# Performance work log

Measured on AMD Instinct MI355X. Metric: run time of the kernel, lower is better.

## Reference

```python
import jax, jax.numpy as jnp
import numpy as np

SEQ_LEN = 16384
IN_DIM = 2048
STATE_DIM = 2048


def setup_inputs() -> dict:
    key = jax.random.key(0)
    k_xs, k_lam, k_win, k_c, k_d = jax.random.split(key, 5)
    xs = jax.random.normal(k_xs, (SEQ_LEN, IN_DIM), dtype=jnp.float32)
    # diagonal state-transition values in (0, 1) for stability
    lam = jax.random.uniform(k_lam, (STATE_DIM,), dtype=jnp.float32)
    w_in = jax.random.normal(k_win, (STATE_DIM, IN_DIM), dtype=jnp.float32) / np.float32(np.sqrt(IN_DIM))
    c_out = jax.random.normal(k_c, (IN_DIM, STATE_DIM), dtype=jnp.float32) / np.float32(np.sqrt(STATE_DIM))
    d_skip = jax.random.normal(k_d, (IN_DIM,), dtype=jnp.float32)
    return {"xs": xs, "lam": lam, "w_in": w_in, "c_out": c_out, "d_skip": d_skip}


def _ssm_cell(a, b):
    # Faithful replication of BaseSSMLayer.ssm_cell (including its use of
    # matrix_pow_i * matrix_pow_i for the first component, exactly as in source).
    matrix_pow_i, bx_i = a
    matrix_pow_j, bx_j = b
    return (matrix_pow_i * matrix_pow_i, matrix_pow_j * bx_i + bx_j)


def reference(xs, lam, w_in, c_out, d_skip):
    seq_len = xs.shape[0]
    # discretize: broadcast diagonal lambda over the sequence -> [L, N]
    lambda_elements = jnp.broadcast_to(lam, (seq_len, lam.shape[0]))
    # preprocess_inputs: vmap(w_in @ x) == xs @ w_in.T  -> [L, N]
    w_in_xs = jnp.einsum('li,ni->ln', xs, w_in)
    _, hs = jax.lax.associative_scan(_ssm_cell, (lambda_elements, w_in_xs))
    # postprocess: y_t = C h_t + D * x_t  -> [L, in_dim]
    return jnp.einsum('ln,on->lo', hs, c_out) + xs * d_skip
```

## Files before the change

### kernel.cpp

```cpp
#include <hip/hip_runtime.h>
#include <hip/hip_bf16.h>

#define SEQ   16384
#define DIM   2048
#define CHUNK 256
#define NCHUNK (SEQ / CHUNK)

typedef __attribute__((ext_vector_type(8))) short  short8;
typedef __attribute__((ext_vector_type(4))) short  short4v;
typedef __attribute__((ext_vector_type(4))) float  floatx4;

static __device__ __forceinline__ float bf2f(short s) {
    return __uint_as_float(((unsigned)(unsigned short)s) << 16);
}
static __device__ __forceinline__ short f2bf(float f) {
    unsigned u = __float_as_uint(f);
    u += 0x7fff + ((u >> 16) & 1);
    return (short)(u >> 16);
}

__global__ void cast_kernel(const float* __restrict__ in, short* __restrict__ out, int n4) {
    int i = blockIdx.x * blockDim.x + threadIdx.x;
    if (i >= n4) return;
    float4 v = ((const float4*)in)[i];
    short4v s;
    s.x = f2bf(v.x); s.y = f2bf(v.y); s.z = f2bf(v.z); s.w = f2bf(v.w);
    ((short4v*)out)[i] = s;
}

template<int FUSE>
__global__ __launch_bounds__(256, 2)
void gemm_bt(const short* __restrict__ A, const short* __restrict__ B,
             short* __restrict__ Cbf, float* __restrict__ Cf,
             const float* __restrict__ xs, const float* __restrict__ dskip)
{
    constexpr int K = DIM;
    __shared__ alignas(16) short As[128 * 32];
    __shared__ alignas(16) short Bs[128 * 32];

    const int tid = threadIdx.x;
    const int m0  = blockIdx.y * 128;
    const int n0  = blockIdx.x * 128;

    const int c0 = tid, c1 = tid + 256;
    const short* ga0 = A + (size_t)(m0 + (c0 >> 2)) * K + (c0 & 3) * 8;
    const short* ga1 = A + (size_t)(m0 + (c1 >> 2)) * K + (c1 & 3) * 8;
    const short* gb0 = B + (size_t)(n0 + (c0 >> 2)) * K + (c0 & 3) * 8;
    const short* gb1 = B + (size_t)(n0 + (c1 >> 2)) * K + (c1 & 3) * 8;
    short* la0 = &As[c0 * 8];
    short* la1 = &As[c1 * 8];
    short* lb0 = &Bs[c0 * 8];
    short* lb1 = &Bs[c1 * 8];

    const int lane = tid & 63;
    const int wv   = tid >> 6;
    const int wm   = (wv >> 1) * 64;
    const int wn   = (wv & 1) * 64;
    const int l16  = lane & 15;
    const int quad = lane >> 4;

    floatx4 acc[4][4] = {};

    for (int kk = 0; kk < K; kk += 32) {
        __builtin_amdgcn_global_load_lds(ga0 + kk, la0, 16, 0, 0);
        __builtin_amdgcn_global_load_lds(ga1 + kk, la1, 16, 0, 0);
        __builtin_amdgcn_global_load_lds(gb0 + kk, lb0, 16, 0, 0);
        __builtin_amdgcn_global_load_lds(gb1 + kk, lb1, 16, 0, 0);
        __syncthreads();

        short8 aV[4], bV[4];
        #pragma unroll
        for (int i = 0; i < 4; i++)
            aV[i] = *(const short8*)&As[(wm + i * 16 + l16) * 32 + quad * 8];
        #pragma unroll
        for (int i = 0; i < 4; i++)
            bV[i] = *(const short8*)&Bs[(wn + i * 16 + l16) * 32 + quad * 8];

        #pragma unroll
        for (int mi = 0; mi < 4; mi++)
            #pragma unroll
            for (int ni = 0; ni < 4; ni++)
                acc[mi][ni] = __builtin_amdgcn_mfma_f32_16x16x32_bf16(
                    aV[mi], bV[ni], acc[mi][ni], 0, 0, 0);
        __syncthreads();
    }

    if (FUSE == 0) {
        #pragma unroll
        for (int mi = 0; mi < 4; mi++) {
            int rb = m0 + wm + mi * 16 + quad * 4;
            #pragma unroll
            for (int ni = 0; ni < 4; ni++) {
                int cc = n0 + wn + ni * 16 + l16;
                #pragma unroll
                for (int r = 0; r < 4; r++)
                    Cbf[(size_t)(rb + r) * DIM + cc] = f2bf(acc[mi][ni][r]);
            }
        }
    } else {
        float dsk[4];
        #pragma unroll
        for (int ni = 0; ni < 4; ni++) dsk[ni] = dskip[n0 + wn + ni * 16 + l16];
        #pragma unroll
        for (int mi = 0; mi < 4; mi++) {
            int rb = m0 + wm + mi * 16 + quad * 4;
            #pragma unroll
            for (int ni = 0; ni < 4; ni++) {
                int cc = n0 + wn + ni * 16 + l16;
                #pragma unroll
                for (int r = 0; r < 4; r++) {
                    size_t idx = (size_t)(rb + r) * DIM + cc;
                    Cf[idx] = acc[mi][ni][r] + xs[idx] * dsk[ni];
                }
            }
        }
    }
}

__global__ void scan_pass1(const short* __restrict__ bx, const float* __restrict__ lam,
                           float* __restrict__ blockLast)
{
    int n     = blockIdx.x * 256 + threadIdx.x;
    int chunk = blockIdx.y;
    float lm  = lam[n];
    const short* p = bx + (size_t)chunk * CHUNK * DIM + n;
    float h = 0.f;
    #pragma unroll 8
    for (int i = 0; i < CHUNK; i++)
        h = fmaf(lm, h, bf2f(p[(size_t)i * DIM]));
    blockLast[(size_t)chunk * DIM + n] = h;
}

__global__ void scan_pass2(float* __restrict__ blockLast, const float* __restrict__ lam)
{
    int n    = blockIdx.x * 256 + threadIdx.x;
    float lm = lam[n];
    float p  = lm;
    #pragma unroll
    for (int i = 0; i < 8; i++) p = p * p;
    float carry = 0.f;
    for (int c = 0; c < NCHUNK; c++) {
        float t = blockLast[(size_t)c * DIM + n];
        blockLast[(size_t)c * DIM + n] = carry;
        carry = fmaf(p, carry, t);
    }
}

__global__ void scan_pass3(short* __restrict__ bxh, const float* __restrict__ lam,
                           const float* __restrict__ carry)
{
    int n     = blockIdx.x * 256 + threadIdx.x;
    int chunk = blockIdx.y;
    float lm  = lam[n];
    float h   = carry[(size_t)chunk * DIM + n];
    short* p  = bxh + (size_t)chunk * CHUNK * DIM + n;
    #pragma unroll 8
    for (int i = 0; i < CHUNK; i++) {
        h = fmaf(lm, h, bf2f(p[(size_t)i * DIM]));
        p[(size_t)i * DIM] = f2bf(h);
    }
}

extern "C" void kernel_launch(void* const* d_in, const int* in_sizes, int n_in,
                              void* d_out, int out_size, void* d_ws, size_t ws_size,
                              hipStream_t stream)
{
    const float* xs    = (const float*)d_in[0];
    const float* lam   = (const float*)d_in[1];
    const float* w_in  = (const float*)d_in[2];
    const float* c_out = (const float*)d_in[3];
    const float* dskip = (const float*)d_in[4];
    float* out = (float*)d_out;

    char*  ws    = (char*)d_ws;
    short* bxh   = (short*)ws;
    short* w_bf  = (short*)(ws + (size_t)64 * 1024 * 1024);
    short* c_bf  = (short*)(ws + (size_t)72 * 1024 * 1024);
    float* blkl  = (float*)(ws + (size_t)80 * 1024 * 1024);
    short* xs_bf = (short*)d_out;

    cast_kernel<<<SEQ * DIM / 4 / 256, 256, 0, stream>>>(xs, xs_bf, SEQ * DIM / 4);
    cast_kernel<<<DIM * DIM / 4 / 256, 256, 0, stream>>>(w_in, w_bf, DIM * DIM / 4);
    cast_kernel<<<DIM * DIM / 4 / 256, 256, 0, stream>>>(c_out, c_bf, DIM * DIM / 4);

    dim3 ggrid(DIM / 128, SEQ / 128);
    gemm_bt<0><<<ggrid, 256, 0, stream>>>(xs_bf, w_bf, bxh, nullptr, nullptr, nullptr);

    dim3 sgrid(DIM / 256, NCHUNK);
    scan_pass1<<<sgrid, 256, 0, stream>>>(bxh, lam, blkl);
    scan_pass2<<<DIM / 256, 256, 0, stream>>>(blkl, lam);
    scan_pass3<<<sgrid, 256, 0, stream>>>(bxh, lam, blkl);

    gemm_bt<1><<<ggrid, 256, 0, stream>>>(bxh, c_bf, nullptr, out, xs, dskip);
}
```

Baseline: 629.3 us.

## Double-buffer GEMM LDS tiles and vectorize chunked scan passes

The GEMM now double-buffers its LDS tiles, issuing the next k-slice's global-to-LDS loads before computing the current one, and drops one barrier per iteration. The three scan passes now have each thread handle four state columns with vectorized bf16 and float4 accesses. The chunk size is halved so the coarser per-thread work still gives enough blocks. Double buffering doubles LDS use per block, and the single-barrier scheme relies on global_load_lds completion being covered by the barrier wait. The scan grid is still small (2x128 blocks).

```diff
diff --git a/kernel.cpp b/kernel.cpp
--- a/kernel.cpp
+++ b/kernel.cpp
@@ -3,7 +3,7 @@
 
 #define SEQ   16384
 #define DIM   2048
-#define CHUNK 256
+#define CHUNK 128
 #define NCHUNK (SEQ / CHUNK)
 
 typedef __attribute__((ext_vector_type(8))) short  short8;
@@ -35,8 +35,9 @@
              const float* __restrict__ xs, const float* __restrict__ dskip)
 {
     constexpr int K = DIM;
-    __shared__ alignas(16) short As[128 * 32];
-    __shared__ alignas(16) short Bs[128 * 32];
+    constexpr int ITERS = K / 32;
+    __shared__ alignas(16) short As[2][128 * 32];
+    __shared__ alignas(16) short Bs[2][128 * 32];
 
     const int tid = threadIdx.x;
     const int m0  = blockIdx.y * 128;
@@ -47,10 +48,6 @@
     const short* ga1 = A + (size_t)(m0 + (c1 >> 2)) * K + (c1 & 3) * 8;
     const short* gb0 = B + (size_t)(n0 + (c0 >> 2)) * K + (c0 & 3) * 8;
     const short* gb1 = B + (size_t)(n0 + (c1 >> 2)) * K + (c1 & 3) * 8;
-    short* la0 = &As[c0 * 8];
-    short* la1 = &As[c1 * 8];
-    short* lb0 = &Bs[c0 * 8];
-    short* lb1 = &Bs[c1 * 8];
 
     const int lane = tid & 63;
     const int wv   = tid >> 6;
@@ -61,20 +58,31 @@
 
     floatx4 acc[4][4] = {};
 
-    for (int kk = 0; kk < K; kk += 32) {
-        __builtin_amdgcn_global_load_lds(ga0 + kk, la0, 16, 0, 0);
-        __builtin_amdgcn_global_load_lds(ga1 + kk, la1, 16, 0, 0);
-        __builtin_amdgcn_global_load_lds(gb0 + kk, lb0, 16, 0, 0);
-        __builtin_amdgcn_global_load_lds(gb1 + kk, lb1, 16, 0, 0);
+    __builtin_amdgcn_global_load_lds(ga0, &As[0][c0 * 8], 16, 0, 0);
+    __builtin_amdgcn_global_load_lds(ga1, &As[0][c1 * 8], 16, 0, 0);
+    __builtin_amdgcn_global_load_lds(gb0, &Bs[0][c0 * 8], 16, 0, 0);
+    __builtin_amdgcn_global_load_lds(gb1, &Bs[0][c1 * 8], 16, 0, 0);
+
+    for (int it = 0; it < ITERS; ++it) {
+        const int cur = it & 1;
         __syncthreads();
 
+        if (it + 1 < ITERS) {
+            const int kk = (it + 1) * 32;
+            const int nxt = cur ^ 1;
+            __builtin_amdgcn_global_load_lds(ga0 + kk, &As[nxt][c0 * 8], 16, 0, 0);
+            __builtin_amdgcn_global_load_lds(ga1 + kk, &As[nxt][c1 * 8], 16, 0, 0);
+            __builtin_amdgcn_global_load_lds(gb0 + kk, &Bs[nxt][c0 * 8], 16, 0, 0);
+            __builtin_amdgcn_global_load_lds(gb1 + kk, &Bs[nxt][c1 * 8], 16, 0, 0);
+        }
+
         short8 aV[4], bV[4];
         #pragma unroll
         for (int i = 0; i < 4; i++)
-            aV[i] = *(const short8*)&As[(wm + i * 16 + l16) * 32 + quad * 8];
+            aV[i] = *(const short8*)&As[cur][(wm + i * 16 + l16) * 32 + quad * 8];
         #pragma unroll
         for (int i = 0; i < 4; i++)
-            bV[i] = *(const short8*)&Bs[(wn + i * 16 + l16) * 32 + quad * 8];
+            bV[i] = *(const short8*)&Bs[cur][(wn + i * 16 + l16) * 32 + quad * 8];
 
         #pragma unroll
         for (int mi = 0; mi < 4; mi++)
@@ -82,7 +90,6 @@
             for (int ni = 0; ni < 4; ni++)
                 acc[mi][ni] = __builtin_amdgcn_mfma_f32_16x16x32_bf16(
                     aV[mi], bV[ni], acc[mi][ni], 0, 0, 0);
-        __syncthreads();
     }
 
     if (FUSE == 0) {
@@ -120,44 +127,62 @@
 __global__ void scan_pass1(const short* __restrict__ bx, const float* __restrict__ lam,
                            float* __restrict__ blockLast)
 {
-    int n     = blockIdx.x * 256 + threadIdx.x;
+    int n     = blockIdx.x * 1024 + threadIdx.x * 4;
     int chunk = blockIdx.y;
-    float lm  = lam[n];
+    float4 lmv = *(const float4*)(lam + n);
+    float lm[4] = {lmv.x, lmv.y, lmv.z, lmv.w};
+    float h[4]  = {0.f, 0.f, 0.f, 0.f};
     const short* p = bx + (size_t)chunk * CHUNK * DIM + n;
-    float h = 0.f;
-    #pragma unroll 8
-    for (int i = 0; i < CHUNK; i++)
-        h = fmaf(lm, h, bf2f(p[(size_t)i * DIM]));
-    blockLast[(size_t)chunk * DIM + n] = h;
+    #pragma unroll 4
+    for (int i = 0; i < CHUNK; i++) {
+        short4v v = *(const short4v*)(p + (size_t)i * DIM);
+        h[0] = fmaf(lm[0], h[0], bf2f(v.x));
+        h[1] = fmaf(lm[1], h[1], bf2f(v.y));
+        h[2] = fmaf(lm[2], h[2], bf2f(v.z));
+        h[3] = fmaf(lm[3], h[3], bf2f(v.w));
+    }
+    *(float4*)(blockLast + (size_t)chunk * DIM + n) = make_float4(h[0], h[1], h[2], h[3]);
 }
 
 __global__ void scan_pass2(float* __restrict__ blockLast, const float* __restrict__ lam)
 {
-    int n    = blockIdx.x * 256 + threadIdx.x;
-    float lm = lam[n];
-    float p  = lm;
+    int n = blockIdx.x * 1024 + threadIdx.x * 4;
+    float4 lmv = *(const float4*)(lam + n);
+    float p0 = lmv.x, p1 = lmv.y, p2 = lmv.z, p3 = lmv.w;
     #pragma unroll
-    for (int i = 0; i < 8; i++) p = p * p;
-    float carry = 0.f;
-    for (int c = 0; c < NCHUNK; c++) {
-        float t = blockLast[(size_t)c * DIM + n];
-        blockLast[(size_t)c * DIM + n] = carry;
-        carry = fmaf(p, carry, t);
+    for (int i = 0; i < 7; i++) { p0 *= p0; p1 *= p1; p2 *= p2; p3 *= p3; }
+    float c[4] = {0.f, 0.f, 0.f, 0.f};
+    for (int ch = 0; ch < NCHUNK; ch++) {
+        float* q = blockLast + (size_t)ch * DIM + n;
+        float4 t = *(const float4*)q;
+        *(float4*)q = make_float4(c[0], c[1], c[2], c[3]);
+        c[0] = fmaf(p0, c[0], t.x);
+        c[1] = fmaf(p1, c[1], t.y);
+        c[2] = fmaf(p2, c[2], t.z);
+        c[3] = fmaf(p3, c[3], t.w);
     }
 }
 
 __global__ void scan_pass3(short* __restrict__ bxh, const float* __restrict__ lam,
                            const float* __restrict__ carry)
 {
-    int n     = blockIdx.x * 256 + threadIdx.x;
+    int n     = blockIdx.x * 1024 + threadIdx.x * 4;
     int chunk = blockIdx.y;
-    float lm  = lam[n];
-    float h   = carry[(size_t)chunk * DIM + n];
-    short* p  = bxh + (size_t)chunk * CHUNK * DIM + n;
-    #pragma unroll 8
+    float4 lmv = *(const float4*)(lam + n);
+    float4 cv  = *(const float4*)(carry + (size_t)chunk * DIM + n);
+    float lm[4] = {lmv.x, lmv.y, lmv.z, lmv.w};
+    float h[4]  = {cv.x, cv.y, cv.z, cv.w};
+    short* p = bxh + (size_t)chunk * CHUNK * DIM + n;
+    #pragma unroll 4
     for (int i = 0; i < CHUNK; i++) {
-        h = fmaf(lm, h, bf2f(p[(size_t)i * DIM]));
-        p[(size_t)i * DIM] = f2bf(h);
+        short4v v = *(const short4v*)(p + (size_t)i * DIM);
+        h[0] = fmaf(lm[0], h[0], bf2f(v.x));
+        h[1] = fmaf(lm[1], h[1], bf2f(v.y));
+        h[2] = fmaf(lm[2], h[2], bf2f(v.z));
+        h[3] = fmaf(lm[3], h[3], bf2f(v.w));
+        short4v o;
+        o.x = f2bf(h[0]); o.y = f2bf(h[1]); o.z = f2bf(h[2]); o.w = f2bf(h[3]);
+        *(short4v*)(p + (size_t)i * DIM) = o;
     }
 }
 
@@ -186,9 +211,9 @@
     dim3 ggrid(DIM / 128, SEQ / 128);
     gemm_bt<0><<<ggrid, 256, 0, stream>>>(xs_bf, w_bf, bxh, nullptr, nullptr, nullptr);
 
-    dim3 sgrid(DIM / 256, NCHUNK);
+    dim3 sgrid(DIM / 1024, NCHUNK);
     scan_pass1<<<sgrid, 256, 0, stream>>>(bxh, lam, blkl);
-    scan_pass2<<<DIM / 256, 256, 0, stream>>>(blkl, lam);
+    scan_pass2<<<DIM / 1024, 256, 0, stream>>>(blkl, lam);
     scan_pass3<<<sgrid, 256, 0, stream>>>(bxh, lam, blkl);
 
     gemm_bt<1><<<ggrid, 256, 0, stream>>>(bxh, c_bf, nullptr, out, xs, dskip);
```

Result: no change. 635.3 us (+1.0%).
